# Performance work log

Measured on AMD Instinct MI355X. Metric: run time of the kernel, lower is better.

The kernel has to match this reference:

```python
import jax, jax.numpy as jnp
import numpy as np
import math

D_KEY = 64
SCALE = math.sqrt(D_KEY)
INF = 1e10  # finite stand-in for the original INF constant
CAUSAL = True
DIAG = False


def setup_inputs() -> dict:
    key = jax.random.key(0)
    kq, kk, kv = jax.random.split(key, 3)
    B, L, D = 16, 2048, D_KEY
    return {
        "query": jax.random.normal(kq, (B, L, D), dtype=jnp.float32),
        "key": jax.random.normal(kk, (B, L, D), dtype=jnp.float32),
        "value": jax.random.normal(kv, (B, L, D), dtype=jnp.float32),
    }


def reference(query, key, value):
    # scores: [B, Lq, Lk]
    scores = jnp.einsum("bqd,bkd->bqk", query, key)
    L = key.shape[1]
    if CAUSAL:
        # subtract INF above the diagonal (strict upper triangle), as in torch triu(1)
        tri = jnp.triu(jnp.full((L, L), INF, dtype=scores.dtype), k=1)
        scores = scores - tri[None, :, :]
    if DIAG:
        # original scatters -INF onto the diagonal along dim 1
        diag_mask = jnp.eye(L, dtype=bool)
        scores = jnp.where(diag_mask[None, :, :], -INF, scores)
    # softmax over keys after scaling; dropout with p=0.0 is identity
    attn = jax.nn.softmax(scores / SCALE, axis=-1)
    return jnp.einsum("bqk,bkd->bqd", attn, value)
```

## Files before the change

### kernel.cpp

```cpp
#include <hip/hip_runtime.h>

typedef __bf16 bf16_t;
typedef __bf16 bf16x4 __attribute__((ext_vector_type(4)));
typedef __bf16 bf16x8 __attribute__((ext_vector_type(8)));
typedef float  f32x4  __attribute__((ext_vector_type(4)));

#define B_SZ  16
#define L_SEQ 2048
#define D_H   64
#define QB    64
#define KB    128
#define NQT   (L_SEQ / QB)

#define QSCALE 0.18033688011112043f

__global__ __launch_bounds__(512, 4)
void attn_pc_kernel(const float* __restrict__ Qg, const float* __restrict__ Kg,
                    const float* __restrict__ Vg, float* __restrict__ Og)
{
    const int lin  = blockIdx.x;
    const int xcd  = lin & 7;
    const int slot = lin >> 3;
    const int half = slot >> 5;
    const int qi   = slot & 31;
    const int b    = xcd * 2 + half;
    const int qt   = half ? qi : (31 - qi);

    const int tid  = threadIdx.x;
    const int wave = tid >> 6;
    const int lane = tid & 63;
    const int lg   = lane >> 4;
    const int lc   = lane & 15;

    __shared__ __align__(16) bf16_t K_lds[2][KB][72];
    __shared__ __align__(16) bf16_t Vt_lds[2][D_H][136];

    const size_t bbase = (size_t)b * L_SEQ * D_H;
    const int nkt = (qt + 2) >> 1;

    if (wave >= 4) {
        const int pt   = tid - 256;
        const int vkb  = pt & 31;
        const int vdg  = pt >> 5;
        const int vpos = ((vkb >> 3) << 5) + ((vkb & 3) << 3) + (((vkb >> 2) & 1) << 2);

        f32x4 kreg[8], vreg[8];

        auto issueK = [&](int kt) {
            const int kbase = kt * KB;
#pragma unroll
            for (int i = 0; i < 8; ++i) {
                const int f = i * 256 + pt;
                const int r = f >> 4, c4 = (f & 15) * 4;
                kreg[i] = *reinterpret_cast<const f32x4*>(Kg + bbase + (size_t)(kbase + r) * D_H + c4);
            }
        };
        auto issueV = [&](int kt) {
            const int kbase = kt * KB;
#pragma unroll
            for (int d2 = 0; d2 < 2; ++d2)
#pragma unroll
                for (int i = 0; i < 4; ++i)
                    vreg[d2 * 4 + i] = *reinterpret_cast<const f32x4*>(
                        Vg + bbase + (size_t)(kbase + vkb * 4 + i) * D_H + (vdg + d2 * 8) * 4);
        };
        auto writeK = [&](int buf) {
#pragma unroll
            for (int i = 0; i < 8; ++i) {
                const int f = i * 256 + pt;
                const int r = f >> 4, c4 = (f & 15) * 4;
                bf16x4 k4 = { (bf16_t)kreg[i][0], (bf16_t)kreg[i][1], (bf16_t)kreg[i][2], (bf16_t)kreg[i][3] };
                *reinterpret_cast<bf16x4*>(&K_lds[buf][r][c4]) = k4;
            }
        };
        auto writeV = [&](int buf) {
#pragma unroll
            for (int d2 = 0; d2 < 2; ++d2) {
                const int db = vdg + d2 * 8;
#pragma unroll
                for (int j = 0; j < 4; ++j) {
                    bf16x4 cj = { (bf16_t)vreg[d2 * 4 + 0][j], (bf16_t)vreg[d2 * 4 + 1][j],
                                  (bf16_t)vreg[d2 * 4 + 2][j], (bf16_t)vreg[d2 * 4 + 3][j] };
                    *reinterpret_cast<bf16x4*>(&Vt_lds[buf][db * 4 + j][vpos]) = cj;
                }
            }
        };

        issueK(0); issueV(0); writeK(0); writeV(0);
        __syncthreads();
        for (int kt = 0; kt < nkt; ++kt) {
            if (kt + 1 < nkt) {
                issueK(kt + 1); issueV(kt + 1);
                writeK((kt + 1) & 1); writeV((kt + 1) & 1);
            }
            __syncthreads();
        }
    } else {
        const int qrow = qt * QB + wave * 16 + lc;
        bf16x8 qa[2];
#pragma unroll
        for (int h = 0; h < 2; ++h) {
            const float* qp = Qg + bbase + (size_t)qrow * D_H + h * 32 + lg * 8;
            const f32x4 f0 = *reinterpret_cast<const f32x4*>(qp);
            const f32x4 f1 = *reinterpret_cast<const f32x4*>(qp + 4);
            bf16x8 a;
#pragma unroll
            for (int j = 0; j < 4; ++j) { a[j] = (bf16_t)(f0[j] * QSCALE); a[4 + j] = (bf16_t)(f1[j] * QSCALE); }
            qa[h] = a;
        }

        f32x4 o[4];
#pragma unroll
        for (int dt = 0; dt < 4; ++dt) o[dt] = (f32x4){0.f, 0.f, 0.f, 0.f};
        float m = -1e30f, l = 0.f;

        __syncthreads();
        for (int kt = 0; kt < nkt; ++kt) {
            const bool last = (kt == nkt - 1);
            const int kbase = kt * KB;
            const int cur   = kt & 1;

            f32x4 sc[8];
            __builtin_amdgcn_s_setprio(1);
#pragma unroll
            for (int n = 0; n < 8; ++n) {
                f32x4 acc = (f32x4){0.f, 0.f, 0.f, 0.f};
#pragma unroll
                for (int h = 0; h < 2; ++h) {
                    const bf16x8 kb = *reinterpret_cast<const bf16x8*>(&K_lds[cur][n * 16 + lc][h * 32 + lg * 8]);
                    acc = __builtin_amdgcn_mfma_f32_16x16x32_bf16(kb, qa[h], acc, 0, 0, 0);
                }
                sc[n] = acc;
            }
            __builtin_amdgcn_s_setprio(0);
            if (last) {
#pragma unroll
                for (int n = 0; n < 8; ++n)
#pragma unroll
                    for (int r = 0; r < 4; ++r)
                        if (kbase + n * 16 + lg * 4 + r > qrow) sc[n][r] = -1e30f;
            }

            float mxp = fmaxf(fmaxf(sc[0][0], sc[0][1]), fmaxf(sc[0][2], sc[0][3]));
#pragma unroll
            for (int n = 1; n < 8; ++n)
                mxp = fmaxf(mxp, fmaxf(fmaxf(sc[n][0], sc[n][1]), fmaxf(sc[n][2], sc[n][3])));
            if (!__all(mxp <= m + 8.0f)) {
                float mx = mxp;
                mx = fmaxf(mx, __shfl_xor(mx, 16));
                mx = fmaxf(mx, __shfl_xor(mx, 32));
                const float mn = fmaxf(m, mx);
                const float alpha = exp2f(m - mn);
                m = mn;
                l *= alpha;
#pragma unroll
                for (int dt = 0; dt < 4; ++dt)
#pragma unroll
                    for (int r = 0; r < 4; ++r) o[dt][r] *= alpha;
            }
            bf16x8 w[4];
            float rs = 0.f;
#pragma unroll
            for (int n = 0; n < 8; ++n) {
                const float p0 = exp2f(sc[n][0] - m), p1 = exp2f(sc[n][1] - m);
                const float p2 = exp2f(sc[n][2] - m), p3 = exp2f(sc[n][3] - m);
                rs += (p0 + p1) + (p2 + p3);
                const int wi = n >> 1, off = (n & 1) * 4;
                w[wi][off + 0] = (bf16_t)p0; w[wi][off + 1] = (bf16_t)p1;
                w[wi][off + 2] = (bf16_t)p2; w[wi][off + 3] = (bf16_t)p3;
            }
            l += rs;

            __builtin_amdgcn_s_setprio(1);
#pragma unroll
            for (int ks = 0; ks < 4; ++ks) {
#pragma unroll
                for (int dt = 0; dt < 4; ++dt) {
                    const bf16x8 vb = *reinterpret_cast<const bf16x8*>(&Vt_lds[cur][dt * 16 + lc][ks * 32 + lg * 8]);
                    o[dt] = __builtin_amdgcn_mfma_f32_16x16x32_bf16(vb, w[ks], o[dt], 0, 0, 0);
                }
            }
            __builtin_amdgcn_s_setprio(0);

            __syncthreads();
        }

        float lr = l;
        lr += __shfl_xor(lr, 16);
        lr += __shfl_xor(lr, 32);
        const float inv = 1.0f / lr;
#pragma unroll
        for (int dt = 0; dt < 4; ++dt) {
            f32x4 val = { o[dt][0] * inv, o[dt][1] * inv, o[dt][2] * inv, o[dt][3] * inv };
            *reinterpret_cast<f32x4*>(Og + bbase + (size_t)qrow * D_H + dt * 16 + lg * 4) = val;
        }
    }
}

extern "C" void kernel_launch(void* const* d_in, const int* in_sizes, int n_in,
                              void* d_out, int out_size, void* d_ws, size_t ws_size,
                              hipStream_t stream)
{
    const float* Q = (const float*)d_in[0];
    const float* K = (const float*)d_in[1];
    const float* V = (const float*)d_in[2];
    float* O = (float*)d_out;
    attn_pc_kernel<<<dim3(NQT * B_SZ), dim3(512), 0, stream>>>(Q, K, V, O);
}
```

Baseline: 33.92 us.

## Switch attention to 32x32x16 MFMA with 256-thread blocks

Replaces the 16x16x32 bf16 MFMA tiles with 32x32x16 tiles, so each compute wave handles 32 query rows. Blocks shrink from 8 waves to 4 (2 compute, 2 producer), and each producer thread loads twice as much K/V per tile. The aim is fewer MFMA issues, fewer LDS fragment reads per FLOP and cheaper row reductions. In exchange each wave holds more live registers, and with fewer waves per block there is less latency hiding and producer bandwidth per tile.

New measurement: 40.63 us. 1.2x slower.

```diff
diff --git a/kernel.cpp b/kernel.cpp
--- a/kernel.cpp
+++ b/kernel.cpp
@@ -4,6 +4,7 @@
 typedef __bf16 bf16x4 __attribute__((ext_vector_type(4)));
 typedef __bf16 bf16x8 __attribute__((ext_vector_type(8)));
 typedef float  f32x4  __attribute__((ext_vector_type(4)));
+typedef float  f32x16 __attribute__((ext_vector_type(16)));
 
 #define B_SZ  16
 #define L_SEQ 2048
@@ -14,9 +15,9 @@
 
 #define QSCALE 0.18033688011112043f
 
-__global__ __launch_bounds__(512, 4)
-void attn_pc_kernel(const float* __restrict__ Qg, const float* __restrict__ Kg,
-                    const float* __restrict__ Vg, float* __restrict__ Og)
+__global__ __launch_bounds__(256, 2)
+void attn_pc32_kernel(const float* __restrict__ Qg, const float* __restrict__ Kg,
+                      const float* __restrict__ Vg, float* __restrict__ Og)
 {
     const int lin  = blockIdx.x;
     const int xcd  = lin & 7;
@@ -29,8 +30,8 @@
     const int tid  = threadIdx.x;
     const int wave = tid >> 6;
     const int lane = tid & 63;
-    const int lg   = lane >> 4;
-    const int lc   = lane & 15;
+    const int lo5  = lane & 31;
+    const int hi   = lane >> 5;
 
     __shared__ __align__(16) bf16_t K_lds[2][KB][72];
     __shared__ __align__(16) bf16_t Vt_lds[2][D_H][136];
@@ -38,19 +39,19 @@
     const size_t bbase = (size_t)b * L_SEQ * D_H;
     const int nkt = (qt + 2) >> 1;
 
-    if (wave >= 4) {
-        const int pt   = tid - 256;
-        const int vkb  = pt & 31;
-        const int vdg  = pt >> 5;
-        const int vpos = ((vkb >> 3) << 5) + ((vkb & 3) << 3) + (((vkb >> 2) & 1) << 2);
-
-        f32x4 kreg[8], vreg[8];
+    if (wave >= 2) {
+        const int pt  = tid - 128;
+        const int vkb = pt & 31;
+        const int db0 = pt >> 5;
+        const int vposb = (vkb >> 2) * 16 + (((vkb >> 1) & 1) << 2) + ((vkb & 1) << 3);
+
+        f32x4 kreg[16], vreg[16];
 
         auto issueK = [&](int kt) {
             const int kbase = kt * KB;
 #pragma unroll
-            for (int i = 0; i < 8; ++i) {
-                const int f = i * 256 + pt;
+            for (int i = 0; i < 16; ++i) {
+                const int f = i * 128 + pt;
                 const int r = f >> 4, c4 = (f & 15) * 4;
                 kreg[i] = *reinterpret_cast<const f32x4*>(Kg + bbase + (size_t)(kbase + r) * D_H + c4);
             }
@@ -58,16 +59,16 @@
         auto issueV = [&](int kt) {
             const int kbase = kt * KB;
 #pragma unroll
-            for (int d2 = 0; d2 < 2; ++d2)
+            for (int t = 0; t < 4; ++t)
 #pragma unroll
                 for (int i = 0; i < 4; ++i)
-                    vreg[d2 * 4 + i] = *reinterpret_cast<const f32x4*>(
-                        Vg + bbase + (size_t)(kbase + vkb * 4 + i) * D_H + (vdg + d2 * 8) * 4);
+                    vreg[t * 4 + i] = *reinterpret_cast<const f32x4*>(
+                        Vg + bbase + (size_t)(kbase + vkb * 4 + i) * D_H + (db0 + 4 * t) * 4);
         };
         auto writeK = [&](int buf) {
 #pragma unroll
-            for (int i = 0; i < 8; ++i) {
-                const int f = i * 256 + pt;
+            for (int i = 0; i < 16; ++i) {
+                const int f = i * 128 + pt;
                 const int r = f >> 4, c4 = (f & 15) * 4;
                 bf16x4 k4 = { (bf16_t)kreg[i][0], (bf16_t)kreg[i][1], (bf16_t)kreg[i][2], (bf16_t)kreg[i][3] };
                 *reinterpret_cast<bf16x4*>(&K_lds[buf][r][c4]) = k4;
@@ -75,13 +76,13 @@
         };
         auto writeV = [&](int buf) {
 #pragma unroll
-            for (int d2 = 0; d2 < 2; ++d2) {
-                const int db = vdg + d2 * 8;
-#pragma unroll
-                for (int j = 0; j < 4; ++j) {
-                    bf16x4 cj = { (bf16_t)vreg[d2 * 4 + 0][j], (bf16_t)vreg[d2 * 4 + 1][j],
-                                  (bf16_t)vreg[d2 * 4 + 2][j], (bf16_t)vreg[d2 * 4 + 3][j] };
-                    *reinterpret_cast<bf16x4*>(&Vt_lds[buf][db * 4 + j][vpos]) = cj;
+            for (int t = 0; t < 4; ++t) {
+                const int db = db0 + 4 * t;
+#pragma unroll
+                for (int jj = 0; jj < 4; ++jj) {
+                    bf16x4 cj = { (bf16_t)vreg[t * 4 + 0][jj], (bf16_t)vreg[t * 4 + 1][jj],
+                                  (bf16_t)vreg[t * 4 + 2][jj], (bf16_t)vreg[t * 4 + 3][jj] };
+                    *reinterpret_cast<bf16x4*>(&Vt_lds[buf][db * 4 + jj][vposb]) = cj;
                 }
             }
         };
@@ -96,11 +97,11 @@
             __syncthreads();
         }
     } else {
-        const int qrow = qt * QB + wave * 16 + lc;
-        bf16x8 qa[2];
-#pragma unroll
-        for (int h = 0; h < 2; ++h) {
-            const float* qp = Qg + bbase + (size_t)qrow * D_H + h * 32 + lg * 8;
+        const int qcol = qt * QB + wave * 32 + lo5;
+        bf16x8 qa[4];
+#pragma unroll
+        for (int h = 0; h < 4; ++h) {
+            const float* qp = Qg + bbase + (size_t)qcol * D_H + h * 16 + hi * 8;
             const f32x4 f0 = *reinterpret_cast<const f32x4*>(qp);
             const f32x4 f1 = *reinterpret_cast<const f32x4*>(qp + 4);
             bf16x8 a;
@@ -109,9 +110,11 @@
             qa[h] = a;
         }
 
-        f32x4 o[4];
-#pragma unroll
-        for (int dt = 0; dt < 4; ++dt) o[dt] = (f32x4){0.f, 0.f, 0.f, 0.f};
+        f32x16 o[2];
+#pragma unroll
+        for (int dt = 0; dt < 2; ++dt)
+#pragma unroll
+            for (int i = 0; i < 16; ++i) o[dt][i] = 0.f;
         float m = -1e30f, l = 0.f;
 
         __syncthreads();
@@ -120,64 +123,67 @@
             const int kbase = kt * KB;
             const int cur   = kt & 1;
 
-            f32x4 sc[8];
+            f32x16 sc[4];
             __builtin_amdgcn_s_setprio(1);
 #pragma unroll
-            for (int n = 0; n < 8; ++n) {
-                f32x4 acc = (f32x4){0.f, 0.f, 0.f, 0.f};
-#pragma unroll
-                for (int h = 0; h < 2; ++h) {
-                    const bf16x8 kb = *reinterpret_cast<const bf16x8*>(&K_lds[cur][n * 16 + lc][h * 32 + lg * 8]);
-                    acc = __builtin_amdgcn_mfma_f32_16x16x32_bf16(kb, qa[h], acc, 0, 0, 0);
+            for (int n = 0; n < 4; ++n) {
+                f32x16 acc;
+#pragma unroll
+                for (int i = 0; i < 16; ++i) acc[i] = 0.f;
+#pragma unroll
+                for (int h = 0; h < 4; ++h) {
+                    const bf16x8 kb = *reinterpret_cast<const bf16x8*>(&K_lds[cur][n * 32 + lo5][h * 16 + hi * 8]);
+                    acc = __builtin_amdgcn_mfma_f32_32x32x16_bf16(kb, qa[h], acc, 0, 0, 0);
                 }
                 sc[n] = acc;
             }
             __builtin_amdgcn_s_setprio(0);
             if (last) {
 #pragma unroll
-                for (int n = 0; n < 8; ++n)
-#pragma unroll
-                    for (int r = 0; r < 4; ++r)
-                        if (kbase + n * 16 + lg * 4 + r > qrow) sc[n][r] = -1e30f;
-            }
-
-            float mxp = fmaxf(fmaxf(sc[0][0], sc[0][1]), fmaxf(sc[0][2], sc[0][3]));
-#pragma unroll
-            for (int n = 1; n < 8; ++n)
-                mxp = fmaxf(mxp, fmaxf(fmaxf(sc[n][0], sc[n][1]), fmaxf(sc[n][2], sc[n][3])));
+                for (int n = 0; n < 4; ++n)
+#pragma unroll
+                    for (int i = 0; i < 16; ++i)
+                        if (kbase + n * 32 + (i & 3) + 8 * (i >> 2) + 4 * hi > qcol) sc[n][i] = -1e30f;
+            }
+
+            float mxp = sc[0][0];
+#pragma unroll
+            for (int n = 0; n < 4; ++n)
+#pragma unroll
+                for (int i = 0; i < 16; ++i) mxp = fmaxf(mxp, sc[n][i]);
             if (!__all(mxp <= m + 8.0f)) {
-                float mx = mxp;
-                mx = fmaxf(mx, __shfl_xor(mx, 16));
-                mx = fmaxf(mx, __shfl_xor(mx, 32));
+                float mx = fmaxf(mxp, __shfl_xor(mxp, 32));
                 const float mn = fmaxf(m, mx);
                 const float alpha = exp2f(m - mn);
                 m = mn;
                 l *= alpha;
 #pragma unroll
-                for (int dt = 0; dt < 4; ++dt)
-#pragma unroll
-                    for (int r = 0; r < 4; ++r) o[dt][r] *= alpha;
-            }
-            bf16x8 w[4];
+                for (int dt = 0; dt < 2; ++dt)
+#pragma unroll
+                    for (int i = 0; i < 16; ++i) o[dt][i] *= alpha;
+            }
             float rs = 0.f;
 #pragma unroll
-            for (int n = 0; n < 8; ++n) {
-                const float p0 = exp2f(sc[n][0] - m), p1 = exp2f(sc[n][1] - m);
-                const float p2 = exp2f(sc[n][2] - m), p3 = exp2f(sc[n][3] - m);
-                rs += (p0 + p1) + (p2 + p3);
-                const int wi = n >> 1, off = (n & 1) * 4;
-                w[wi][off + 0] = (bf16_t)p0; w[wi][off + 1] = (bf16_t)p1;
-                w[wi][off + 2] = (bf16_t)p2; w[wi][off + 3] = (bf16_t)p3;
-            }
+            for (int n = 0; n < 4; ++n)
+#pragma unroll
+                for (int i = 0; i < 16; ++i) {
+                    const float p = exp2f(sc[n][i] - m);
+                    rs += p;
+                    sc[n][i] = p;
+                }
             l += rs;
 
             __builtin_amdgcn_s_setprio(1);
 #pragma unroll
-            for (int ks = 0; ks < 4; ++ks) {
-#pragma unroll
-                for (int dt = 0; dt < 4; ++dt) {
-                    const bf16x8 vb = *reinterpret_cast<const bf16x8*>(&Vt_lds[cur][dt * 16 + lc][ks * 32 + lg * 8]);
-                    o[dt] = __builtin_amdgcn_mfma_f32_16x16x32_bf16(vb, w[ks], o[dt], 0, 0, 0);
+            for (int s = 0; s < 8; ++s) {
+                bf16x8 w;
+#pragma unroll
+                for (int j = 0; j < 8; ++j)
+                    w[j] = (bf16_t)sc[s >> 1][(((2 * (s & 1)) + (j >> 2)) << 2) | (j & 3)];
+#pragma unroll
+                for (int dt = 0; dt < 2; ++dt) {
+                    const bf16x8 vb = *reinterpret_cast<const bf16x8*>(&Vt_lds[cur][dt * 32 + lo5][s * 16 + hi * 8]);
+                    o[dt] = __builtin_amdgcn_mfma_f32_32x32x16_bf16(vb, w, o[dt], 0, 0, 0);
                 }
             }
             __builtin_amdgcn_s_setprio(0);
@@ -185,15 +191,16 @@
             __syncthreads();
         }
 
-        float lr = l;
-        lr += __shfl_xor(lr, 16);
-        lr += __shfl_xor(lr, 32);
+        float lr = l + __shfl_xor(l, 32);
         const float inv = 1.0f / lr;
 #pragma unroll
-        for (int dt = 0; dt < 4; ++dt) {
-            f32x4 val = { o[dt][0] * inv, o[dt][1] * inv, o[dt][2] * inv, o[dt][3] * inv };
-            *reinterpret_cast<f32x4*>(Og + bbase + (size_t)qrow * D_H + dt * 16 + lg * 4) = val;
-        }
+        for (int dt = 0; dt < 2; ++dt)
+#pragma unroll
+            for (int g = 0; g < 4; ++g) {
+                f32x4 val = { o[dt][4 * g + 0] * inv, o[dt][4 * g + 1] * inv,
+                              o[dt][4 * g + 2] * inv, o[dt][4 * g + 3] * inv };
+                *reinterpret_cast<f32x4*>(Og + bbase + (size_t)qcol * D_H + dt * 32 + 8 * g + 4 * hi) = val;
+            }
     }
 }
 
@@ -205,5 +212,5 @@
     const float* K = (const float*)d_in[1];
     const float* V = (const float*)d_in[2];
     float* O = (float*)d_out;
-    attn_pc_kernel<<<dim3(NQT * B_SZ), dim3(512), 0, stream>>>(Q, K, V, O);
+    attn_pc32_kernel<<<dim3(NQT * B_SZ), dim3(256), 0, stream>>>(Q, K, V, O);
 }
```
